# Kernel tuning notes

Hardware: AMD Instinct MI355X
Metric: run time of the kernel (lower is better)

The kernel has to match this reference:

```python
import jax, jax.numpy as jnp
import numpy as np

L = 6          # encoder layers
D = 512        # d_model
H = 8          # heads
HD = D // H    # head_dim = 64
M = 64         # num random features (num_orf)
DFF = 2048     # feedforward dim
B = 16         # batch
S = 2048       # sequence length (hw)
NQ = 100       # query_embed rows (unused by encoder)
EPS = 1e-5
STAB = 1e-3    # relu kernel numerical stabilizer


def _ln(x, s, b):
    mu = jnp.mean(x, axis=-1, keepdims=True)
    var = jnp.mean((x - mu) ** 2, axis=-1, keepdims=True)
    return (x - mu) / jnp.sqrt(var + EPS) * s + b


def _performer_attn(x_qk, v_in, Wqkv, bqkv, Wo, bo, w):
    # x_qk, v_in: [S,B,D]; Wqkv: [3D,D]; w: [M,HD]
    q = x_qk @ Wqkv[:D].T + bqkv[:D]
    k = x_qk @ Wqkv[D:2 * D].T + bqkv[D:2 * D]
    v = v_in @ Wqkv[2 * D:].T + bqkv[2 * D:]
    q = q.reshape(S, B, H, HD)
    k = k.reshape(S, B, H, HD)
    v = v.reshape(S, B, H, HD)
    ratio = 1.0 / (M ** 0.25)  # 1/sqrt(sqrt(m))
    qp = jax.nn.relu(ratio * jnp.einsum('sbhd,md->sbhm', q, w)) + STAB
    kp = jax.nn.relu(ratio * jnp.einsum('sbhd,md->sbhm', k, w)) + STAB
    kv = jnp.einsum('sbhm,sbhd->bhmd', kp, v)              # O(n) linear attention
    num = jnp.einsum('sbhm,bhmd->sbhd', qp, kv)
    den = jnp.einsum('sbhm,bhm->sbh', qp, kp.sum(axis=0))[..., None]
    out = (num / den).reshape(S, B, D)
    return out @ Wo.T + bo


def setup_inputs() -> dict:
    key = jax.random.key(0)
    ks = jax.random.split(key, 8)
    src = jax.random.normal(ks[0], (B, S, D), jnp.float32)
    query_embed = jax.random.normal(ks[1], (NQ, D), jnp.float32)
    pos_embed = jax.random.normal(ks[2], (B, S, D), jnp.float32)
    in_proj_w = jax.random.normal(ks[3], (L, 3 * D, D), jnp.float32) * (D ** -0.5)
    in_proj_b = jnp.zeros((L, 3 * D), jnp.float32)
    out_w = jax.random.normal(ks[4], (L, D, D), jnp.float32) * (D ** -0.5)
    out_b = jnp.zeros((L, D), jnp.float32)
    lin1_w = jax.random.normal(ks[5], (L, DFF, D), jnp.float32) * (D ** -0.5)
    lin1_b = jnp.zeros((L, DFF), jnp.float32)
    lin2_w = jax.random.normal(ks[6], (L, D, DFF), jnp.float32) * (DFF ** -0.5)
    lin2_b = jnp.zeros((L, D), jnp.float32)
    norm1_s = jnp.ones((L, D), jnp.float32)
    norm1_b = jnp.zeros((L, D), jnp.float32)
    norm2_s = jnp.ones((L, D), jnp.float32)
    norm2_b = jnp.zeros((L, D), jnp.float32)
    # gaussian orthogonal random matrices (scaling=0): Q^T from QR, rows rescaled by chi norms
    rng = np.random.default_rng(0)
    ws = []
    for _ in range(L):
        q, _ = np.linalg.qr(rng.standard_normal((HD, HD)))
        mult = np.linalg.norm(rng.standard_normal((M, HD)), axis=1)
        ws.append(np.diag(mult) @ q.T)
    w_orf = jnp.asarray(np.stack(ws), jnp.float32)
    return dict(src=src, query_embed=query_embed, pos_embed=pos_embed,
                in_proj_w=in_proj_w, in_proj_b=in_proj_b, out_w=out_w, out_b=out_b,
                lin1_w=lin1_w, lin1_b=lin1_b, lin2_w=lin2_w, lin2_b=lin2_b,
                norm1_s=norm1_s, norm1_b=norm1_b, norm2_s=norm2_s, norm2_b=norm2_b,
                w_orf=w_orf)


def reference(src, query_embed, pos_embed, in_proj_w, in_proj_b, out_w, out_b,
              lin1_w, lin1_b, lin2_w, lin2_b, norm1_s, norm1_b, norm2_s, norm2_b,
              w_orf):
    del query_embed  # only encoder memory is returned
    x = jnp.transpose(src, (1, 0, 2))        # [S,B,D]
    pos = jnp.transpose(pos_embed, (1, 0, 2))
    for i in range(L):  # post-norm encoder layers (dropout inactive in eval)
        qk = x + pos
        a = _performer_attn(qk, x, in_proj_w[i], in_proj_b[i], out_w[i], out_b[i], w_orf[i])
        x = _ln(x + a, norm1_s[i], norm1_b[i])
        f = jax.nn.relu(x @ lin1_w[i].T + lin1_b[i]) @ lin2_w[i].T + lin2_b[i]
        x = _ln(x + f, norm2_s[i], norm2_b[i])
    return x  # memory: [S,B,D]
```

## Files before the change

### kernel.cpp

```cpp
#include <hip/hip_runtime.h>

typedef unsigned short u16;
typedef unsigned int   u32;
typedef __attribute__((ext_vector_type(8))) short short8;
typedef __attribute__((ext_vector_type(4))) float f32x4;

constexpr int Dc   = 512;
constexpr int Lc   = 6;
constexpr int Bc   = 16;
constexpr int Sc   = 2048;
constexpr int Rc   = Sc * Bc;
constexpr float RATIO = 0.3535533905932738f;
constexpr float STABc = 1e-3f;
constexpr float EPSc  = 1e-5f;

__device__ __forceinline__ u32 pk2(float lo, float hi) {
    u32 a = __float_as_uint(lo), b = __float_as_uint(hi);
    a = (a + 0x7FFFu + ((a >> 16) & 1u)) >> 16;
    b = (b + 0x7FFFu + ((b >> 16) & 1u)) & 0xFFFF0000u;
    return a | b;
}
__device__ __forceinline__ u16 f2bh(float f) {
    u32 u = __float_as_uint(f);
    return (u16)((u + 0x7FFFu + ((u >> 16) & 1u)) >> 16);
}
__device__ __forceinline__ float b2f(u16 u) { return __uint_as_float(((u32)u) << 16); }

__global__ __launch_bounds__(256)
void sentinel_kernel(float* O, int n4) {
    int i = blockIdx.x * 256 + threadIdx.x;
    if (i < n4) {
        float4 v = make_float4(12345.f, 12345.f, 12345.f, 12345.f);
        *reinterpret_cast<float4*>(O + (size_t)i * 4) = v;
    }
}

__global__ __launch_bounds__(256)
void zero_kernel(float* p, int n4) {
    int i = blockIdx.x * 256 + threadIdx.x;
    if (i < n4) {
        float4 z = make_float4(0.f, 0.f, 0.f, 0.f);
        *reinterpret_cast<float4*>(p + (size_t)i * 4) = z;
    }
}

__global__ __launch_bounds__(256)
void wconv_kernel(const float* __restrict__ src, u16* __restrict__ dst, int n8) {
    int i = blockIdx.x * 256 + threadIdx.x;
    if (i >= n8) return;
    size_t base = (size_t)i * 8;
    float4 a = *reinterpret_cast<const float4*>(src + base);
    float4 b = *reinterpret_cast<const float4*>(src + base + 4);
    uint4 o;
    o.x = pk2(a.x, a.y); o.y = pk2(a.z, a.w);
    o.z = pk2(b.x, b.y); o.w = pk2(b.z, b.w);
    *reinterpret_cast<uint4*>(dst + base) = o;
}

__global__ __launch_bounds__(256)
void xp_kernel(const float* __restrict__ X, const float* __restrict__ POS,
               u16* __restrict__ XP) {
    size_t i = (size_t)blockIdx.x * 256 + threadIdx.x;
    size_t base = i * 8;
    float4 x0 = *reinterpret_cast<const float4*>(X + base);
    float4 x1 = *reinterpret_cast<const float4*>(X + base + 4);
    float4 p0 = *reinterpret_cast<const float4*>(POS + base);
    float4 p1 = *reinterpret_cast<const float4*>(POS + base + 4);
    uint4 o;
    o.x = pk2(x0.x + p0.x, x0.y + p0.y);
    o.y = pk2(x0.z + p0.z, x0.w + p0.w);
    o.z = pk2(x1.x + p1.x, x1.y + p1.y);
    o.w = pk2(x1.z + p1.z, x1.w + p1.w);
    *reinterpret_cast<uint4*>(XP + base) = o;
}

__global__ __launch_bounds__(256)
void xb_kernel(const float* __restrict__ X, u16* __restrict__ XB) {
    size_t i = (size_t)blockIdx.x * 256 + threadIdx.x;
    size_t base = i * 8;
    float4 x0 = *reinterpret_cast<const float4*>(X + base);
    float4 x1 = *reinterpret_cast<const float4*>(X + base + 4);
    uint4 o;
    o.x = pk2(x0.x, x0.y); o.y = pk2(x0.z, x0.w);
    o.z = pk2(x1.x, x1.y); o.w = pk2(x1.z, x1.w);
    *reinterpret_cast<uint4*>(XB + base) = o;
}

__global__ __launch_bounds__(256)
void weff_kernel(const float* __restrict__ Wqkv, const float* __restrict__ bqkv,
                 const float* __restrict__ worf,
                 u16* __restrict__ WeffQ, u16* __restrict__ WeffK,
                 float* __restrict__ beffQ, float* __restrict__ beffK) {
    __shared__ float wl[64][64];
    __shared__ float ql[64][68];
    __shared__ float kl[64][68];
    int cc = blockIdx.x, h = blockIdx.y;
    int tid = threadIdx.x;
    for (int i = tid; i < 4096; i += 256) wl[i >> 6][i & 63] = worf[i];
    for (int i = tid; i < 4096; i += 256) {
        int d = i >> 6, c = i & 63;
        ql[d][c] = Wqkv[(size_t)(h * 64 + d) * 512 + cc * 64 + c];
        kl[d][c] = Wqkv[(size_t)(512 + h * 64 + d) * 512 + cc * 64 + c];
    }
    __syncthreads();
    int m = tid >> 2, c0 = (tid & 3) * 16;
    float acc[16];
    #pragma unroll
    for (int j = 0; j < 16; ++j) acc[j] = 0.f;
    for (int d = 0; d < 64; ++d) {
        float wv = wl[m][d];
        #pragma unroll
        for (int j = 0; j < 16; ++j) acc[j] = fmaf(wv, ql[d][c0 + j], acc[j]);
    }
    for (int j = 0; j < 16; ++j)
        WeffQ[(size_t)(h * 64 + m) * 512 + cc * 64 + c0 + j] = f2bh(RATIO * acc[j]);
    #pragma unroll
    for (int j = 0; j < 16; ++j) acc[j] = 0.f;
    for (int d = 0; d < 64; ++d) {
        float wv = wl[m][d];
        #pragma unroll
        for (int j = 0; j < 16; ++j) acc[j] = fmaf(wv, kl[d][c0 + j], acc[j]);
    }
    for (int j = 0; j < 16; ++j)
        WeffK[(size_t)(h * 64 + m) * 512 + cc * 64 + c0 + j] = f2bh(RATIO * acc[j]);
    if (cc == 0 && tid < 64) {
        float bq = 0.f, bk = 0.f;
        for (int d = 0; d < 64; ++d) {
            bq = fmaf(wl[tid][d], bqkv[h * 64 + d], bq);
            bk = fmaf(wl[tid][d], bqkv[512 + h * 64 + d], bk);
        }
        beffQ[h * 64 + tid] = RATIO * bq;
        beffK[h * 64 + tid] = RATIO * bk;
    }
}

template <int MODE, bool ABF16, bool WBF16>
__global__ __launch_bounds__(256)
void gemm_mfma(const void* __restrict__ Av, int lda,
               const void* __restrict__ Wv, int ldw,
               const float* __restrict__ bias, const float* __restrict__ res,
               void* __restrict__ Cv, int ldc, int K) {
    constexpr int LP = 40;
    constexpr bool CB16 = (MODE == 0 || MODE == 1 || MODE == 4);
    __shared__ short As[128 * LP];
    __shared__ short Bs[128 * LP];
    int tid = threadIdx.x;
    int lane = tid & 63, wv = tid >> 6;
    int wr = wv >> 1, wc = wv & 1;
    int row0 = blockIdx.y * 128, col0 = blockIdx.x * 128;

    int srow = tid >> 1;
    int sks  = (tid & 1) << 4;
    int arow = row0 + srow;

    f32x4 acc[4][4];
    #pragma unroll
    for (int mi = 0; mi < 4; ++mi)
        #pragma unroll
        for (int ni = 0; ni < 4; ++ni)
            acc[mi][ni] = (f32x4){0.f, 0.f, 0.f, 0.f};

    int rl = lane & 15;
    int kg = (lane >> 4) * 8;

    for (int k0 = 0; k0 < K; k0 += 32) {
        uint4 qa0, qa1, qb0, qb1;
        if (ABF16) {
            const u16* Ap = (const u16*)Av + (size_t)arow * lda + sks;
            qa0 = *reinterpret_cast<const uint4*>(Ap + k0);
            qa1 = *reinterpret_cast<const uint4*>(Ap + k0 + 8);
        } else {
            const float* Ap = (const float*)Av + (size_t)arow * lda + sks;
            float4 a0 = *reinterpret_cast<const float4*>(Ap + k0);
            float4 a1 = *reinterpret_cast<const float4*>(Ap + k0 + 4);
            float4 a2 = *reinterpret_cast<const float4*>(Ap + k0 + 8);
            float4 a3 = *reinterpret_cast<const float4*>(Ap + k0 + 12);
            qa0.x = pk2(a0.x, a0.y); qa0.y = pk2(a0.z, a0.w);
            qa0.z = pk2(a1.x, a1.y); qa0.w = pk2(a1.z, a1.w);
            qa1.x = pk2(a2.x, a2.y); qa1.y = pk2(a2.z, a2.w);
            qa1.z = pk2(a3.x, a3.y); qa1.w = pk2(a3.z, a3.w);
        }
        if (WBF16) {
            const u16* Wp = (const u16*)Wv + (size_t)(col0 + srow) * ldw + sks;
            qb0 = *reinterpret_cast<const uint4*>(Wp + k0);
            qb1 = *reinterpret_cast<const uint4*>(Wp + k0 + 8);
        } else {
            const float* Wp = (const float*)Wv + (size_t)(col0 + srow) * ldw + sks;
            float4 b0 = *reinterpret_cast<const float4*>(Wp + k0);
            float4 b1 = *reinterpret_cast<const float4*>(Wp + k0 + 4);
            float4 b2 = *reinterpret_cast<const float4*>(Wp + k0 + 8);
            float4 b3 = *reinterpret_cast<const float4*>(Wp + k0 + 12);
            qb0.x = pk2(b0.x, b0.y); qb0.y = pk2(b0.z, b0.w);
            qb0.z = pk2(b1.x, b1.y); qb0.w = pk2(b1.z, b1.w);
            qb1.x = pk2(b2.x, b2.y); qb1.y = pk2(b2.z, b2.w);
            qb1.z = pk2(b3.x, b3.y); qb1.w = pk2(b3.z, b3.w);
        }
        __syncthreads();
        *reinterpret_cast<uint4*>(&As[srow * LP + sks])     = qa0;
        *reinterpret_cast<uint4*>(&As[srow * LP + sks + 8]) = qa1;
        *reinterpret_cast<uint4*>(&Bs[srow * LP + sks])     = qb0;
        *reinterpret_cast<uint4*>(&Bs[srow * LP + sks + 8]) = qb1;
        __syncthreads();
        short8 af[4], bf[4];
        #pragma unroll
        for (int mi = 0; mi < 4; ++mi)
            af[mi] = *reinterpret_cast<const short8*>(&As[(wr * 64 + mi * 16 + rl) * LP + kg]);
        #pragma unroll
        for (int ni = 0; ni < 4; ++ni)
            bf[ni] = *reinterpret_cast<const short8*>(&Bs[(wc * 64 + ni * 16 + rl) * LP + kg]);
        #pragma unroll
        for (int mi = 0; mi < 4; ++mi)
            #pragma unroll
            for (int ni = 0; ni < 4; ++ni)
                acc[mi][ni] = __builtin_amdgcn_mfma_f32_16x16x32_bf16(
                    af[mi], bf[ni], acc[mi][ni], 0, 0, 0);
    }

    int orb = row0 + wr * 64 + (lane >> 4) * 4;
    int ocb = col0 + wc * 64 + rl;
    float bv[4];
    #pragma unroll
    for (int ni = 0; ni < 4; ++ni)
        bv[ni] = (MODE != 3) ? bias[ocb + ni * 16] : 0.f;
    #pragma unroll
    for (int mi = 0; mi < 4; ++mi) {
        #pragma unroll
        for (int j = 0; j < 4; ++j) {
            int orow = orb + mi * 16 + j;
            size_t base = (size_t)orow * ldc + ocb;
            #pragma unroll
            for (int ni = 0; ni < 4; ++ni) {
                float v = acc[mi][ni][j] + bv[ni];
                if (MODE == 1) v = fmaxf(v, 0.f);
                if (MODE == 4) v = fmaxf(v, 0.f) + STABc;
                size_t off = base + ni * 16;
                if (MODE == 2) v += res[off];
                if (MODE == 3) v += ((float*)Cv)[off];
                if (CB16) ((u16*)Cv)[off] = f2bh(v);
                else      ((float*)Cv)[off] = v;
            }
        }
    }
}

__global__ __launch_bounds__(256)
void kv_split(const u16* __restrict__ KQP, const u16* __restrict__ V,
              float* __restrict__ KV, float* __restrict__ KSUM) {
    __shared__ u16 kpl[128 * 64];
    __shared__ u16 vl[128 * 64];
    int bh = blockIdx.x, sc = blockIdx.y;
    int b = bh >> 3, h = bh & 7;
    int tid = threadIdx.x;
    int d = tid & 63, mg = tid >> 6;
    float acc[16], ks[16];
    #pragma unroll
    for (int i = 0; i < 16; ++i) { acc[i] = 0.f; ks[i] = 0.f; }
    size_t rowbase = (size_t)b * Sc + sc * 512;
    for (int c = 0; c < 4; ++c) {
        __syncthreads();
        for (int i = tid; i < 1024; i += 256) {
            int row = i >> 3, c8 = (i & 7) * 8;
            size_t r = rowbase + c * 128 + row;
            *reinterpret_cast<uint4*>(&kpl[row * 64 + c8]) =
                *reinterpret_cast<const uint4*>(KQP + r * 1024 + h * 64 + c8);
            *reinterpret_cast<uint4*>(&vl[row * 64 + c8]) =
                *reinterpret_cast<const uint4*>(V + r * 512 + h * 64 + c8);
        }
        __syncthreads();
        for (int s = 0; s < 128; ++s) {
            float vv = b2f(vl[s * 64 + d]);
            #pragma unroll
            for (int i = 0; i < 16; ++i) {
                float kp = b2f(kpl[s * 64 + mg * 16 + i]);
                acc[i] = fmaf(kp, vv, acc[i]);
                ks[i] += kp;
            }
        }
    }
    float* kvp = KV + (size_t)bh * 4096;
    #pragma unroll
    for (int i = 0; i < 16; ++i)
        atomicAdd(&kvp[(mg * 16 + i) * 64 + d], acc[i]);
    if (d == 0) {
        #pragma unroll
        for (int i = 0; i < 16; ++i)
            atomicAdd(&KSUM[bh * 64 + mg * 16 + i], ks[i]);
    }
}

__global__ __launch_bounds__(256)
void numden_mfma(const u16* __restrict__ KQP, const float* __restrict__ KVg,
                 const float* __restrict__ KSUM, u16* __restrict__ OUT) {
    constexpr int LP = 72;
    __shared__ short Asm[128 * LP];
    __shared__ short BT[64 * LP];
    __shared__ float ksl[64];
    __shared__ float dsm[128][2];
    int h  = blockIdx.x;
    int row0 = blockIdx.y * 128;
    int b  = row0 >> 11;
    int tid = threadIdx.x;
    int lane = tid & 63, w = tid >> 6;

    const float* kvp = KVg + ((size_t)(b * 8 + h)) * 4096;
    for (int i = tid; i < 4096; i += 256) {
        int m = i >> 6, d = i & 63;
        BT[d * LP + m] = (short)f2bh(kvp[i]);
    }
    if (tid < 64) ksl[tid] = KSUM[(b * 8 + h) * 64 + tid];
    {
        int rr = tid >> 1;
        int cc = (tid & 1) * 32;
        const u16* qp = KQP + (size_t)(row0 + rr) * 1024 + 512 + h * 64 + cc;
        #pragma unroll
        for (int q = 0; q < 4; ++q)
            *reinterpret_cast<uint4*>(&Asm[rr * LP + cc + q * 8]) =
                *reinterpret_cast<const uint4*>(qp + q * 8);
    }
    __syncthreads();

    {
        int rr = tid >> 1, half = tid & 1;
        const short* ap = &Asm[rr * LP + half * 32];
        float pden = 0.f;
        #pragma unroll
        for (int m = 0; m < 32; ++m)
            pden = fmaf(b2f((u16)ap[m]), ksl[half * 32 + m], pden);
        dsm[rr][half] = pden;
    }
    __syncthreads();

    int rl = lane & 15, kq = (lane >> 4) * 8;
    f32x4 acc[2][4];
    #pragma unroll
    for (int mi = 0; mi < 2; ++mi)
        #pragma unroll
        for (int ni = 0; ni < 4; ++ni) acc[mi][ni] = (f32x4){0.f, 0.f, 0.f, 0.f};
    #pragma unroll
    for (int kst = 0; kst < 2; ++kst) {
        int kg = kst * 32 + kq;
        short8 a0 = *reinterpret_cast<const short8*>(&Asm[(w * 32 + rl) * LP + kg]);
        short8 a1 = *reinterpret_cast<const short8*>(&Asm[(w * 32 + 16 + rl) * LP + kg]);
        short8 bf[4];
        #pragma unroll
        for (int ni = 0; ni < 4; ++ni)
            bf[ni] = *reinterpret_cast<const short8*>(&BT[(ni * 16 + rl) * LP + kg]);
        #pragma unroll
        for (int ni = 0; ni < 4; ++ni) {
            acc[0][ni] = __builtin_amdgcn_mfma_f32_16x16x32_bf16(a0, bf[ni], acc[0][ni], 0, 0, 0);
            acc[1][ni] = __builtin_amdgcn_mfma_f32_16x16x32_bf16(a1, bf[ni], acc[1][ni], 0, 0, 0);
        }
    }
    #pragma unroll
    for (int mi = 0; mi < 2; ++mi) {
        #pragma unroll
        for (int j = 0; j < 4; ++j) {
            int lr = w * 32 + mi * 16 + (lane >> 4) * 4 + j;
            int row = row0 + lr;
            float inv = 1.f / (dsm[lr][0] + dsm[lr][1]);
            #pragma unroll
            for (int ni = 0; ni < 4; ++ni)
                OUT[(size_t)row * Dc + h * 64 + ni * 16 + rl] =
                    f2bh(acc[mi][ni][j] * inv);
        }
    }
}

template <bool PERM>
__global__ __launch_bounds__(256)
void ln_kernel(const float* __restrict__ X, const float* __restrict__ Sg,
               const float* __restrict__ Bg, float* __restrict__ O) {
    int lane = threadIdx.x & 63, w = threadIdx.x >> 6;
    size_t r = (size_t)blockIdx.x * 4 + w;
    const float* xr = X + r * Dc;
    float v[8];
    *reinterpret_cast<float4*>(&v[0]) = *reinterpret_cast<const float4*>(xr + lane * 4);
    *reinterpret_cast<float4*>(&v[4]) = *reinterpret_cast<const float4*>(xr + 256 + lane * 4);
    float sum = 0.f;
    #pragma unroll
    for (int i = 0; i < 8; ++i) sum += v[i];
    #pragma unroll
    for (int off = 32; off >= 1; off >>= 1) sum += __shfl_xor(sum, off);
    float mu = sum * (1.f / Dc);
    float sq = 0.f;
    #pragma unroll
    for (int i = 0; i < 8; ++i) { float dd = v[i] - mu; sq += dd * dd; }
    #pragma unroll
    for (int off = 32; off >= 1; off >>= 1) sq += __shfl_xor(sq, off);
    float rstd = rsqrtf(sq * (1.f / Dc) + EPSc);
    float s[8], b[8];
    *reinterpret_cast<float4*>(&s[0]) = *reinterpret_cast<const float4*>(Sg + lane * 4);
    *reinterpret_cast<float4*>(&s[4]) = *reinterpret_cast<const float4*>(Sg + 256 + lane * 4);
    *reinterpret_cast<float4*>(&b[0]) = *reinterpret_cast<const float4*>(Bg + lane * 4);
    *reinterpret_cast<float4*>(&b[4]) = *reinterpret_cast<const float4*>(Bg + 256 + lane * 4);
    float o[8];
    #pragma unroll
    for (int i = 0; i < 8; ++i) o[i] = (v[i] - mu) * rstd * s[i] + b[i];
    size_t rd = PERM ? ((size_t)(r & (Sc - 1)) * Bc + (r >> 11)) : r;
    float* orow = O + rd * Dc;
    *reinterpret_cast<float4*>(orow + lane * 4) = *reinterpret_cast<const float4*>(&o[0]);
    *reinterpret_cast<float4*>(orow + 256 + lane * 4) = *reinterpret_cast<const float4*>(&o[4]);
}

__global__ __launch_bounds__(256)
void ln2f_kernel(float* __restrict__ X, const float* __restrict__ Sg,
                 const float* __restrict__ Bg, const float* __restrict__ POS,
                 u16* __restrict__ XP, u16* __restrict__ XB) {
    int lane = threadIdx.x & 63, w = threadIdx.x >> 6;
    size_t r = (size_t)blockIdx.x * 4 + w;
    float* xr = X + r * Dc;
    float v[8];
    *reinterpret_cast<float4*>(&v[0]) = *reinterpret_cast<const float4*>(xr + lane * 4);
    *reinterpret_cast<float4*>(&v[4]) = *reinterpret_cast<const float4*>(xr + 256 + lane * 4);
    float sum = 0.f;
    #pragma unroll
    for (int i = 0; i < 8; ++i) sum += v[i];
    #pragma unroll
    for (int off = 32; off >= 1; off >>= 1) sum += __shfl_xor(sum, off);
    float mu = sum * (1.f / Dc);
    float sq = 0.f;
    #pragma unroll
    for (int i = 0; i < 8; ++i) { float dd = v[i] - mu; sq += dd * dd; }
    #pragma unroll
    for (int off = 32; off >= 1; off >>= 1) sq += __shfl_xor(sq, off);
    float rstd = rsqrtf(sq * (1.f / Dc) + EPSc);
    float s[8], b[8];
    *reinterpret_cast<float4*>(&s[0]) = *reinterpret_cast<const float4*>(Sg + lane * 4);
    *reinterpret_cast<float4*>(&s[4]) = *reinterpret_cast<const float4*>(Sg + 256 + lane * 4);
    *reinterpret_cast<float4*>(&b[0]) = *reinterpret_cast<const float4*>(Bg + lane * 4);
    *reinterpret_cast<float4*>(&b[4]) = *reinterpret_cast<const float4*>(Bg + 256 + lane * 4);
    float p[8];
    *reinterpret_cast<float4*>(&p[0]) = *reinterpret_cast<const float4*>(POS + r * Dc + lane * 4);
    *reinterpret_cast<float4*>(&p[4]) = *reinterpret_cast<const float4*>(POS + r * Dc + 256 + lane * 4);
    float o[8];
    #pragma unroll
    for (int i = 0; i < 8; ++i) o[i] = (v[i] - mu) * rstd * s[i] + b[i];
    *reinterpret_cast<float4*>(xr + lane * 4)       = *reinterpret_cast<const float4*>(&o[0]);
    *reinterpret_cast<float4*>(xr + 256 + lane * 4) = *reinterpret_cast<const float4*>(&o[4]);
    uint2 xb0, xb1, xp0, xp1;
    xb0.x = pk2(o[0], o[1]); xb0.y = pk2(o[2], o[3]);
    xb1.x = pk2(o[4], o[5]); xb1.y = pk2(o[6], o[7]);
    xp0.x = pk2(o[0] + p[0], o[1] + p[1]); xp0.y = pk2(o[2] + p[2], o[3] + p[3]);
    xp1.x = pk2(o[4] + p[4], o[5] + p[5]); xp1.y = pk2(o[6] + p[6], o[7] + p[7]);
    *reinterpret_cast<uint2*>(XB + r * Dc + lane * 4)       = xb0;
    *reinterpret_cast<uint2*>(XB + r * Dc + 256 + lane * 4) = xb1;
    *reinterpret_cast<uint2*>(XP + r * Dc + lane * 4)       = xp0;
    *reinterpret_cast<uint2*>(XP + r * Dc + 256 + lane * 4) = xp1;
}

extern "C" void kernel_launch(void* const* d_in, const int* in_sizes, int n_in,
                              void* d_out, int out_size, void* d_ws, size_t ws_size,
                              hipStream_t stream) {
    (void)in_sizes; (void)n_in; (void)out_size;
    const float* src   = (const float*)d_in[0];
    const float* pos   = (const float*)d_in[2];
    const float* ipw   = (const float*)d_in[3];
    const float* ipb   = (const float*)d_in[4];
    const float* outw  = (const float*)d_in[5];
    const float* outb  = (const float*)d_in[6];
    const float* l1w   = (const float*)d_in[7];
    const float* l1b   = (const float*)d_in[8];
    const float* l2w   = (const float*)d_in[9];
    const float* l2b   = (const float*)d_in[10];
    const float* n1s   = (const float*)d_in[11];
    const float* n1b   = (const float*)d_in[12];
    const float* n2s   = (const float*)d_in[13];
    const float* n2b   = (const float*)d_in[14];
    const float* worf  = (const float*)d_in[15];
    float* out = (float*)d_out;

    const size_t RD = (size_t)Rc * Dc;
    const size_t NEED = RD * 4 + RD * 4 + (size_t)128 * 4096 * 4 + 8192 * 4
                      + (size_t)Rc * 8 * 4 + 2 * 262144 * 2 + 2 * 512 * 4;
    if (ws_size < NEED) {
        sentinel_kernel<<<(Rc * Dc / 4 + 255) / 256, 256, 0, stream>>>(out, Rc * Dc / 4);
        return;
    }
    char* p = (char*)d_ws;
    float* X    = (float*)p;  p += RD * 4;
    float* B2f  = (float*)p;  p += RD * 4;
    float* KV   = (float*)p;  p += (size_t)128 * 4096 * 4;
    float* KSUM = (float*)p;  p += 8192 * 4;
    p += (size_t)Rc * 8 * 4;
    u16*  WeffKQ = (u16*)p;   p += 2 * 262144 * 2;
    float* beffKQ = (float*)p;

    u16*  B2u  = (u16*)B2f;
    u16*  XPu  = B2u;
    u16*  Vu   = B2u + RD;
    u16*  AOu  = B2u + RD;
    u16*  H1u  = B2u;
    u16*  OutU = (u16*)out;
    u16*  XB2u = OutU;
    u16*  KQPu = OutU;
    float* T1f = out;
    u16*  XBu  = OutU;
    u16*  W1bD = OutU + RD;
    u16*  W2bD = OutU + RD + 1048576;

    dim3 blk(256);
    dim3 g512(4, Rc / 128);
    dim3 g1024(8, Rc / 128);
    dim3 g2048(16, Rc / 128);
    const int nz4 = (128 * 4096 + 8192) / 4;

    for (int i = 0; i < Lc; ++i) {
        const float* w_qkv = ipw + (size_t)i * 1536 * 512;
        const float* b_qkv = ipb + (size_t)i * 1536;
        const float* w_v  = w_qkv + (size_t)1024 * 512;
        const float* b_v  = b_qkv + 1024;
        const float* w_o  = outw + (size_t)i * 512 * 512;
        const float* b_o  = outb + (size_t)i * 512;
        const float* w_1  = l1w + (size_t)i * 2048 * 512;
        const float* b_1  = l1b + (size_t)i * 2048;
        const float* w_2  = l2w + (size_t)i * 512 * 2048;
        const float* b_2  = l2b + (size_t)i * 512;
        const float* wo_i = worf + (size_t)i * 4096;

        weff_kernel<<<dim3(8, 8), blk, 0, stream>>>(
            w_qkv, b_qkv, wo_i, WeffKQ + 262144, WeffKQ, beffKQ + 512, beffKQ);

        if (i == 0) {
            hipMemcpyAsync(X, src, RD * 4, hipMemcpyDeviceToDevice, stream);
            xb_kernel<<<(int)(RD / 8 / 256), blk, 0, stream>>>(X, XB2u);
            xp_kernel<<<(int)(RD / 8 / 256), blk, 0, stream>>>(X, pos, XPu);
        }

        gemm_mfma<0, true, false><<<g512, blk, 0, stream>>>(
            XB2u, 512, w_v, 512, b_v, nullptr, Vu, 512, 512);
        gemm_mfma<4, true, true><<<g1024, blk, 0, stream>>>(
            XPu, 512, WeffKQ, 512, beffKQ, nullptr, KQPu, 1024, 512);
        zero_kernel<<<(nz4 + 255) / 256, blk, 0, stream>>>(KV, nz4);
        kv_split<<<dim3(128, 4), blk, 0, stream>>>(KQPu, Vu, KV, KSUM);
        numden_mfma<<<dim3(8, Rc / 128), blk, 0, stream>>>(KQPu, KV, KSUM, AOu);
        gemm_mfma<2, true, false><<<g512, blk, 0, stream>>>(
            AOu, 512, w_o, 512, b_o, X, T1f, 512, 512);
        ln_kernel<false><<<Rc / 4, blk, 0, stream>>>(T1f, n1s + i * 512, n1b + i * 512, X);
        xb_kernel<<<(int)(RD / 8 / 256), blk, 0, stream>>>(X, XBu);
        wconv_kernel<<<(1048576 / 8 + 255) / 256, blk, 0, stream>>>(w_1, W1bD, 1048576 / 8);
        wconv_kernel<<<(1048576 / 8 + 255) / 256, blk, 0, stream>>>(w_2, W2bD, 1048576 / 8);
        gemm_mfma<1, true, true><<<g2048, blk, 0, stream>>>(
            XBu, 512, W1bD, 512, b_1, nullptr, H1u, 2048, 512);
        gemm_mfma<2, true, true><<<g512, blk, 0, stream>>>(
            H1u, 2048, W2bD, 2048, b_2, X, X, 512, 2048);
        if (i == Lc - 1)
            ln_kernel<true><<<Rc / 4, blk, 0, stream>>>(X, n2s + i * 512, n2b + i * 512, out);
        else
            ln2f_kernel<<<Rc / 4, blk, 0, stream>>>(X, n2s + i * 512, n2b + i * 512,
                                                    pos, XPu, XB2u);
    }
}
```

Before: 3.715 ms.

## Load GEMM tiles directly into LDS and pre-convert V/O weights to bf16

Replaces the templated GEMM with a bf16-only version that stages A and W tiles with global_load_lds (direct global-to-LDS DMA), removing the register round-trip and the fp32-to-bf16 packing in the inner loop. The V and output-projection weights are now converted to bf16 once per layer into spare workspace, so every GEMM takes bf16 operands. The cost is two extra small conversion launches per layer. The LDS tiles drop their padding, which may raise bank conflicts on the fragment reads, and the loop is still single-buffered with two barriers per step.

After: 3.400 ms. 1.09x faster.

```diff
diff --git a/kernel.cpp b/kernel.cpp
--- a/kernel.cpp
+++ b/kernel.cpp
@@ -25,6 +25,12 @@
     return (u16)((u + 0x7FFFu + ((u >> 16) & 1u)) >> 16);
 }
 __device__ __forceinline__ float b2f(u16 u) { return __uint_as_float(((u32)u) << 16); }
+
+__device__ __forceinline__ void glds16(const u16* g, u16* l) {
+    __builtin_amdgcn_global_load_lds(
+        (const __attribute__((address_space(1))) u32*)g,
+        (__attribute__((address_space(3))) u32*)l, 16, 0, 0);
+}
 
 __global__ __launch_bounds__(256)
 void sentinel_kernel(float* O, int n4) {
@@ -134,24 +140,30 @@
     }
 }
 
-template <int MODE, bool ABF16, bool WBF16>
-__global__ __launch_bounds__(256)
-void gemm_mfma(const void* __restrict__ Av, int lda,
-               const void* __restrict__ Wv, int ldw,
-               const float* __restrict__ bias, const float* __restrict__ res,
-               void* __restrict__ Cv, int ldc, int K) {
-    constexpr int LP = 40;
+template <int MODE>
+__global__ __launch_bounds__(256)
+void gemm_bb(const u16* __restrict__ A, int lda,
+             const u16* __restrict__ W, int ldw,
+             const float* __restrict__ bias, const float* __restrict__ res,
+             void* __restrict__ Cv, int ldc, int K) {
     constexpr bool CB16 = (MODE == 0 || MODE == 1 || MODE == 4);
-    __shared__ short As[128 * LP];
-    __shared__ short Bs[128 * LP];
+    __shared__ u16 As[128 * 32];
+    __shared__ u16 Bs[128 * 32];
     int tid = threadIdx.x;
     int lane = tid & 63, wv = tid >> 6;
     int wr = wv >> 1, wc = wv & 1;
     int row0 = blockIdx.y * 128, col0 = blockIdx.x * 128;
 
-    int srow = tid >> 1;
-    int sks  = (tid & 1) << 4;
-    int arow = row0 + srow;
+    int srow  = wv * 32 + (lane >> 2);
+    int skofs = (lane & 3) * 8;
+    const u16* Ap0 = A + (size_t)(row0 + srow) * lda + skofs;
+    const u16* Ap1 = A + (size_t)(row0 + srow + 16) * lda + skofs;
+    const u16* Wp0 = W + (size_t)(col0 + srow) * ldw + skofs;
+    const u16* Wp1 = W + (size_t)(col0 + srow + 16) * ldw + skofs;
+    u16* AsD0 = &As[(wv * 32) * 32];
+    u16* AsD1 = &As[(wv * 32 + 16) * 32];
+    u16* BsD0 = &Bs[(wv * 32) * 32];
+    u16* BsD1 = &Bs[(wv * 32 + 16) * 32];
 
     f32x4 acc[4][4];
     #pragma unroll
@@ -164,50 +176,19 @@
     int kg = (lane >> 4) * 8;
 
     for (int k0 = 0; k0 < K; k0 += 32) {
-        uint4 qa0, qa1, qb0, qb1;
-        if (ABF16) {
-            const u16* Ap = (const u16*)Av + (size_t)arow * lda + sks;
-            qa0 = *reinterpret_cast<const uint4*>(Ap + k0);
-            qa1 = *reinterpret_cast<const uint4*>(Ap + k0 + 8);
-        } else {
-            const float* Ap = (const float*)Av + (size_t)arow * lda + sks;
-            float4 a0 = *reinterpret_cast<const float4*>(Ap + k0);
-            float4 a1 = *reinterpret_cast<const float4*>(Ap + k0 + 4);
-            float4 a2 = *reinterpret_cast<const float4*>(Ap + k0 + 8);
-            float4 a3 = *reinterpret_cast<const float4*>(Ap + k0 + 12);
-            qa0.x = pk2(a0.x, a0.y); qa0.y = pk2(a0.z, a0.w);
-            qa0.z = pk2(a1.x, a1.y); qa0.w = pk2(a1.z, a1.w);
-            qa1.x = pk2(a2.x, a2.y); qa1.y = pk2(a2.z, a2.w);
-            qa1.z = pk2(a3.x, a3.y); qa1.w = pk2(a3.z, a3.w);
-        }
-        if (WBF16) {
-            const u16* Wp = (const u16*)Wv + (size_t)(col0 + srow) * ldw + sks;
-            qb0 = *reinterpret_cast<const uint4*>(Wp + k0);
-            qb1 = *reinterpret_cast<const uint4*>(Wp + k0 + 8);
-        } else {
-            const float* Wp = (const float*)Wv + (size_t)(col0 + srow) * ldw + sks;
-            float4 b0 = *reinterpret_cast<const float4*>(Wp + k0);
-            float4 b1 = *reinterpret_cast<const float4*>(Wp + k0 + 4);
-            float4 b2 = *reinterpret_cast<const float4*>(Wp + k0 + 8);
-            float4 b3 = *reinterpret_cast<const float4*>(Wp + k0 + 12);
-            qb0.x = pk2(b0.x, b0.y); qb0.y = pk2(b0.z, b0.w);
-            qb0.z = pk2(b1.x, b1.y); qb0.w = pk2(b1.z, b1.w);
-            qb1.x = pk2(b2.x, b2.y); qb1.y = pk2(b2.z, b2.w);
-            qb1.z = pk2(b3.x, b3.y); qb1.w = pk2(b3.z, b3.w);
-        }
         __syncthreads();
-        *reinterpret_cast<uint4*>(&As[srow * LP + sks])     = qa0;
-        *reinterpret_cast<uint4*>(&As[srow * LP + sks + 8]) = qa1;
-        *reinterpret_cast<uint4*>(&Bs[srow * LP + sks])     = qb0;
-        *reinterpret_cast<uint4*>(&Bs[srow * LP + sks + 8]) = qb1;
+        glds16(Ap0 + k0, AsD0);
+        glds16(Ap1 + k0, AsD1);
+        glds16(Wp0 + k0, BsD0);
+        glds16(Wp1 + k0, BsD1);
         __syncthreads();
         short8 af[4], bf[4];
         #pragma unroll
         for (int mi = 0; mi < 4; ++mi)
-            af[mi] = *reinterpret_cast<const short8*>(&As[(wr * 64 + mi * 16 + rl) * LP + kg]);
+            af[mi] = *reinterpret_cast<const short8*>(&As[(wr * 64 + mi * 16 + rl) * 32 + kg]);
         #pragma unroll
         for (int ni = 0; ni < 4; ++ni)
-            bf[ni] = *reinterpret_cast<const short8*>(&Bs[(wc * 64 + ni * 16 + rl) * LP + kg]);
+            bf[ni] = *reinterpret_cast<const short8*>(&Bs[(wc * 64 + ni * 16 + rl) * 32 + kg]);
         #pragma unroll
         for (int mi = 0; mi < 4; ++mi)
             #pragma unroll
@@ -481,6 +462,8 @@
     float* B2f  = (float*)p;  p += RD * 4;
     float* KV   = (float*)p;  p += (size_t)128 * 4096 * 4;
     float* KSUM = (float*)p;  p += 8192 * 4;
+    u16*  WVb   = (u16*)p;
+    u16*  WOb   = WVb + 262144;
     p += (size_t)Rc * 8 * 4;
     u16*  WeffKQ = (u16*)p;   p += 2 * 262144 * 2;
     float* beffKQ = (float*)p;
@@ -519,6 +502,8 @@
 
         weff_kernel<<<dim3(8, 8), blk, 0, stream>>>(
             w_qkv, b_qkv, wo_i, WeffKQ + 262144, WeffKQ, beffKQ + 512, beffKQ);
+        wconv_kernel<<<(262144 / 8 + 255) / 256, blk, 0, stream>>>(w_v, WVb, 262144 / 8);
+        wconv_kernel<<<(262144 / 8 + 255) / 256, blk, 0, stream>>>(w_o, WOb, 262144 / 8);
 
         if (i == 0) {
             hipMemcpyAsync(X, src, RD * 4, hipMemcpyDeviceToDevice, stream);
@@ -526,22 +511,22 @@
             xp_kernel<<<(int)(RD / 8 / 256), blk, 0, stream>>>(X, pos, XPu);
         }
 
-        gemm_mfma<0, true, false><<<g512, blk, 0, stream>>>(
-            XB2u, 512, w_v, 512, b_v, nullptr, Vu, 512, 512);
-        gemm_mfma<4, true, true><<<g1024, blk, 0, stream>>>(
+        gemm_bb<0><<<g512, blk, 0, stream>>>(
+            XB2u, 512, WVb, 512, b_v, nullptr, Vu, 512, 512);
+        gemm_bb<4><<<g1024, blk, 0, stream>>>(
             XPu, 512, WeffKQ, 512, beffKQ, nullptr, KQPu, 1024, 512);
         zero_kernel<<<(nz4 + 255) / 256, blk, 0, stream>>>(KV, nz4);
         kv_split<<<dim3(128, 4), blk, 0, stream>>>(KQPu, Vu, KV, KSUM);
         numden_mfma<<<dim3(8, Rc / 128), blk, 0, stream>>>(KQPu, KV, KSUM, AOu);
-        gemm_mfma<2, true, false><<<g512, blk, 0, stream>>>(
-            AOu, 512, w_o, 512, b_o, X, T1f, 512, 512);
+        gemm_bb<2><<<g512, blk, 0, stream>>>(
+            AOu, 512, WOb, 512, b_o, X, T1f, 512, 512);
         ln_kernel<false><<<Rc / 4, blk, 0, stream>>>(T1f, n1s + i * 512, n1b + i * 512, X);
         xb_kernel<<<(int)(RD / 8 / 256), blk, 0, stream>>>(X, XBu);
         wconv_kernel<<<(1048576 / 8 + 255) / 256, blk, 0, stream>>>(w_1, W1bD, 1048576 / 8);
         wconv_kernel<<<(1048576 / 8 + 255) / 256, blk, 0, stream>>>(w_2, W2bD, 1048576 / 8);
-        gemm_mfma<1, true, true><<<g2048, blk, 0, stream>>>(
+        gemm_bb<1><<<g2048, blk, 0, stream>>>(
             XBu, 512, W1bD, 512, b_1, nullptr, H1u, 2048, 512);
-        gemm_mfma<2, true, true><<<g512, blk, 0, stream>>>(
+        gemm_bb<2><<<g512, blk, 0, stream>>>(
             H1u, 2048, W2bD, 2048, b_2, X, X, 512, 2048);
         if (i == Lc - 1)
             ln_kernel<true><<<Rc / 4, blk, 0, stream>>>(X, n2s + i * 512, n2b + i * 512, out);
```
